# Performance work log

Measured on AMD Instinct MI355X. Metric: run time of the kernel, lower is better.

## Reference

```python
import jax, jax.numpy as jnp
import numpy as np

RADIUS = 2  # module init kwarg


def _lga(cost, weights, r):
    """One local-guided-aggregation pass.
    cost:    [B, D, H, W]
    weights: [B, 3*K*K, H, W], K = 2r+1; group 0/1/2 weight disparity d-1/d/d+1.
    """
    B, D, H, W = cost.shape
    K = 2 * r + 1
    # zero-pad: disparity by 1 (for d-1 / d+1), spatial by r (window)
    cp = jnp.pad(cost, ((0, 0), (1, 1), (r, r), (r, r)))
    w = weights.reshape(B, 3, K * K, H, W)
    out = jnp.zeros_like(cost)
    for idx in range(K * K):
        i, j = idx // K, idx % K
        # window view: cp[:, :, y+i, x+j] == cost[:, :, y+i-r, x+j-r]
        win = cp[:, :, i:i + H, j:j + W]          # [B, D+2, H, W]
        out = out + (w[:, 0, idx][:, None] * win[:, 0:D]        # cost[d-1]
                     + w[:, 1, idx][:, None] * win[:, 1:D + 1]  # cost[d]
                     + w[:, 2, idx][:, None] * win[:, 2:D + 2]) # cost[d+1]
    return out


def setup_inputs() -> dict:
    key = jax.random.key(0)
    k1, k2 = jax.random.split(key)
    B, D, H, W = 2, 64, 384, 768
    K = 2 * RADIUS + 1
    input1 = jax.random.normal(k1, (B, D, H, W), dtype=jnp.float32)
    # aggregation stays numerically tame (mimics normalized guidance)
    input2 = jax.random.uniform(k2, (B, 3 * K * K, H, W), dtype=jnp.float32) * (1.0 / (3 * K * K))
    return {"input1": input1, "input2": input2}


def reference(input1, input2):
    out = input1
    for _ in range(3):  # LGA3 = three sequential LGA passes, same weights
        out = _lga(out, input2, RADIUS)
    return out
```

## Files before the change

kernel.cpp:

```cpp
#include <hip/hip_runtime.h>


#define B_ 2
#define D_ 64
#define H_ 384
#define W_ 768
static constexpr int HW    = H_ * W_;
static constexpr int DPT   = 8;
static constexpr int NTY   = D_ / DPT;
static constexpr int WT    = 64;
static constexpr int HSEG  = 8;
static constexpr int RITER = HSEG + 4;
static constexpr int LROW  = 72;
static constexpr int LPL   = 66;
static constexpr int NCH_C = 18;

__device__ __forceinline__ void gld_lds16(const float* g, float* l) {
  __builtin_amdgcn_global_load_lds((const __attribute__((address_space(1))) unsigned int*)g,
                                   (__attribute__((address_space(3))) unsigned int*)l,
                                   16, 0, 0);
}

__global__ __launch_bounds__(512, 1) void lga_pass(const float* __restrict__ src,
                                                   const float* __restrict__ wts,
                                                   float* __restrict__ dst) {
  __shared__ float cl[2][LPL * LROW];

  const int tx = threadIdx.x;
  const int ty = threadIdx.y;
  const int w0 = blockIdx.x * WT, w = w0 + tx;
  const int hs = blockIdx.y * HSEG;
  const int b  = blockIdx.z;
  const int d0 = ty * DPT;

  const float* sb  = src + (size_t)b * D_ * HW;
  const float* wtb = wts + (size_t)b * 75 * HW;

  const bool has_lo = (d0 > 0);
  const bool has_hi = (d0 + DPT < D_);
  bool wok[5];
#pragma unroll
  for (int j = 0; j < 5; ++j) wok[j] = (unsigned)(w + j - 2) < (unsigned)W_;

  {
    const int h0 = hs - 2;
    if (h0 >= 0) {
#pragma unroll
      for (int q = 0; q < 3; ++q) {
        const int c = ty + q * 8;
        if (c < NCH_C) {
          const int G = c * 64 + tx;
          const int d = G / NCH_C;
          const int k = G - d * NCH_C;
          long idx = (long)d * HW + (long)h0 * W_ + (w0 - 4) + (k << 2);
          idx = idx < 0 ? 0 : idx;
          const long mx = (long)D_ * HW - 4;
          idx = idx > mx ? mx : idx;
          gld_lds16(sb + idx, &cl[0][LROW + c * 256]);
        }
      }
    }
  }
  __syncthreads();

  float acc[5][DPT];
#pragma unroll
  for (int s = 0; s < 5; ++s)
#pragma unroll
    for (int k = 0; k < DPT; ++k) acc[s][k] = 0.f;

  int n = 0;
#pragma unroll 1
  for (int r = 0; r < RITER; ++r) {
    float W[75];
#pragma unroll
    for (int s = 0; s < 5; ++s) {
      if ((unsigned)(r - 4 + s) < (unsigned)HSEG) {
        const int o     = hs + r - 4 + s;
        const int ib    = (4 - s) * 5;
        const float* wr = wtb + (size_t)o * W_;
#pragma unroll
        for (int g = 0; g < 3; ++g)
#pragma unroll
          for (int j = 0; j < 5; ++j)
            W[s * 15 + g * 5 + j] = wr[(size_t)(ib + j + 25 * g) * HW + w];
      }
    }

    if (r + 1 < RITER) {
      const int h_nx = hs - 2 + r + 1;
      if ((unsigned)h_nx < (unsigned)H_) {
#pragma unroll
        for (int q = 0; q < 3; ++q) {
          const int c = ty + q * 8;
          if (c < NCH_C) {
            const int G = c * 64 + tx;
            const int d = G / NCH_C;
            const int k = G - d * NCH_C;
            long idx = (long)d * HW + (long)h_nx * W_ + (w0 - 4) + (k << 2);
            idx = idx < 0 ? 0 : idx;
            const long mx = (long)D_ * HW - 4;
            idx = idx > mx ? mx : idx;
            gld_lds16(sb + idx, &cl[n ^ 1][LROW + c * 256]);
          }
        }
      }
    }

    const int  h_in = hs - 2 + r;
    const bool hv   = (unsigned)h_in < (unsigned)H_;
    float vv[5][DPT + 2];
    if (hv) {
      const float* vbase = cl[n] + d0 * LROW + tx + 2;
#pragma unroll
      for (int j = 0; j < 5; ++j)
#pragma unroll
        for (int m = 0; m < DPT + 2; ++m) {
          const float v = vbase[m * LROW + j];
          bool ok = wok[j];
          if (m == 0)       ok = ok && has_lo;
          if (m == DPT + 1) ok = ok && has_hi;
          vv[j][m] = ok ? v : 0.f;
        }
    }

#pragma unroll
    for (int s = 0; s < 5; ++s) {
      if (hv && (unsigned)(r - 4 + s) < (unsigned)HSEG) {
#pragma unroll
        for (int j = 0; j < 5; ++j)
#pragma unroll
          for (int k = 0; k < DPT; ++k)
            acc[s][k] = fmaf(W[s * 15 + j],      vv[j][k],
                        fmaf(W[s * 15 + 5 + j],  vv[j][k + 1],
                        fmaf(W[s * 15 + 10 + j], vv[j][k + 2], acc[s][k])));
      }
    }

    if (r >= 4) {
      const int o = hs + r - 4;
#pragma unroll
      for (int k = 0; k < DPT; ++k) {
        float* dp = dst + (((size_t)b * D_ + d0 + k) * H_ + o) * W_;
        dp[w] = acc[0][k];
      }
    }

#pragma unroll
    for (int s = 0; s < 4; ++s)
#pragma unroll
      for (int k = 0; k < DPT; ++k) acc[s][k] = acc[s + 1][k];
#pragma unroll
    for (int k = 0; k < DPT; ++k) acc[4][k] = 0.f;

    __syncthreads();
    n ^= 1;
  }
}

extern "C" void kernel_launch(void* const* d_in, const int* in_sizes, int n_in,
                              void* d_out, int out_size, void* d_ws, size_t ws_size,
                              hipStream_t stream) {
  const float* cost = (const float*)d_in[0];
  const float* wts  = (const float*)d_in[1];
  float* out = (float*)d_out;
  float* ws  = (float*)d_ws;

  dim3 grid(W_ / WT, H_ / HSEG, B_);
  dim3 block(WT, NTY);

  lga_pass<<<grid, block, 0, stream>>>(cost, wts, out);
  lga_pass<<<grid, block, 0, stream>>>(out, wts, ws);
  lga_pass<<<grid, block, 0, stream>>>(ws, wts, out);
}
```

Before: 640.3 us.

## Triple-buffer cost-row LDS staging with counted vmcnt waits instead of syncthreads

Replaces double-buffered LDS staging of cost rows with a three-buffer ring that prefetches two rows ahead. Every thread now issues exactly three loads per row, with dummy loads landing in a spare slot, so fixed vmcnt values can be waited on. A raw s_barrier after a partial vmcnt wait replaces the full __syncthreads drain. This is meant to hide global-load latency behind the FMA work, at the cost of more LDS, redundant clamped loads at the edges, and fragile manual waitcnt accounting.

New measurement: 771.4 us. 20.5% more time.

```diff
diff --git a/kernel.cpp b/kernel.cpp
--- a/kernel.cpp
+++ b/kernel.cpp
@@ -12,8 +12,8 @@
 static constexpr int HSEG  = 8;
 static constexpr int RITER = HSEG + 4;
 static constexpr int LROW  = 72;
-static constexpr int LPL   = 66;
 static constexpr int NCH_C = 18;
+static constexpr int LBUF  = LROW + 19 * 256;
 
 __device__ __forceinline__ void gld_lds16(const float* g, float* l) {
   __builtin_amdgcn_global_load_lds((const __attribute__((address_space(1))) unsigned int*)g,
@@ -24,7 +24,7 @@
 __global__ __launch_bounds__(512, 1) void lga_pass(const float* __restrict__ src,
                                                    const float* __restrict__ wts,
                                                    float* __restrict__ dst) {
-  __shared__ float cl[2][LPL * LROW];
+  __shared__ float cl[3][LBUF];
 
   const int tx = threadIdx.x;
   const int ty = threadIdx.y;
@@ -42,26 +42,28 @@
 #pragma unroll
   for (int j = 0; j < 5; ++j) wok[j] = (unsigned)(w + j - 2) < (unsigned)W_;
 
-  {
-    const int h0 = hs - 2;
-    if (h0 >= 0) {
+  auto stage_c = [&](float* buf, int h_in) {
 #pragma unroll
-      for (int q = 0; q < 3; ++q) {
-        const int c = ty + q * 8;
-        if (c < NCH_C) {
-          const int G = c * 64 + tx;
-          const int d = G / NCH_C;
-          const int k = G - d * NCH_C;
-          long idx = (long)d * HW + (long)h0 * W_ + (w0 - 4) + (k << 2);
-          idx = idx < 0 ? 0 : idx;
-          const long mx = (long)D_ * HW - 4;
-          idx = idx > mx ? mx : idx;
-          gld_lds16(sb + idx, &cl[0][LROW + c * 256]);
-        }
-      }
+    for (int q = 0; q < 3; ++q) {
+      const int c    = ty + q * 8;
+      const bool real = (c < NCH_C);
+      const int cc   = real ? c : NCH_C;
+      const int cg   = real ? c : 0;
+      const int G    = cg * 64 + tx;
+      const int d    = G / NCH_C;
+      const int k    = G - d * NCH_C;
+      long idx = (long)d * HW + (long)h_in * W_ + (w0 - 4) + (k << 2);
+      idx = idx < 0 ? 0 : idx;
+      const long mx = (long)D_ * HW - 4;
+      idx = idx > mx ? mx : idx;
+      gld_lds16(sb + idx, &buf[LROW + cc * 256]);
     }
-  }
-  __syncthreads();
+  };
+
+  auto clampH = [](int h) { return h < 0 ? 0 : (h >= H_ ? H_ - 1 : h); };
+
+  stage_c(cl[0], clampH(hs - 2));
+  stage_c(cl[1], clampH(hs - 1));
 
   float acc[5][DPT];
 #pragma unroll
@@ -69,9 +71,13 @@
 #pragma unroll
     for (int k = 0; k < DPT; ++k) acc[s][k] = 0.f;
 
-  int n = 0;
 #pragma unroll 1
   for (int r = 0; r < RITER; ++r) {
+    if (r <= 4) { asm volatile("s_waitcnt vmcnt(3)" ::: "memory"); }
+    else        { asm volatile("s_waitcnt vmcnt(11)" ::: "memory"); }
+    __builtin_amdgcn_s_barrier();
+    asm volatile("" ::: "memory");
+
     float W[75];
 #pragma unroll
     for (int s = 0; s < 5; ++s) {
@@ -87,31 +93,13 @@
       }
     }
 
-    if (r + 1 < RITER) {
-      const int h_nx = hs - 2 + r + 1;
-      if ((unsigned)h_nx < (unsigned)H_) {
-#pragma unroll
-        for (int q = 0; q < 3; ++q) {
-          const int c = ty + q * 8;
-          if (c < NCH_C) {
-            const int G = c * 64 + tx;
-            const int d = G / NCH_C;
-            const int k = G - d * NCH_C;
-            long idx = (long)d * HW + (long)h_nx * W_ + (w0 - 4) + (k << 2);
-            idx = idx < 0 ? 0 : idx;
-            const long mx = (long)D_ * HW - 4;
-            idx = idx > mx ? mx : idx;
-            gld_lds16(sb + idx, &cl[n ^ 1][LROW + c * 256]);
-          }
-        }
-      }
-    }
+    stage_c(cl[(r + 2) % 3], clampH(hs - 2 + r + 2));
 
     const int  h_in = hs - 2 + r;
     const bool hv   = (unsigned)h_in < (unsigned)H_;
     float vv[5][DPT + 2];
     if (hv) {
-      const float* vbase = cl[n] + d0 * LROW + tx + 2;
+      const float* vbase = cl[r % 3] + d0 * LROW + tx + 2;
 #pragma unroll
       for (int j = 0; j < 5; ++j)
 #pragma unroll
@@ -152,9 +140,6 @@
       for (int k = 0; k < DPT; ++k) acc[s][k] = acc[s + 1][k];
 #pragma unroll
     for (int k = 0; k < DPT; ++k) acc[4][k] = 0.f;
-
-    __syncthreads();
-    n ^= 1;
   }
 }
 
```
